# Kernel optimization log

Hardware: AMD Instinct MI355X
Metric: run time of the kernel (lower is better)

The kernel has to match this reference:

```python
import math
import jax, jax.numpy as jnp
import numpy as np

PS = 16   # patch_size
HD = 8    # hidden_dim in SigmaPredictor


def _bsp(x):
    # BoundedSoftplus(beta=1, threshold=6, eps=1e-6)
    return jnp.minimum(jax.nn.softplus(x), 6.0) + 1e-6


def _attn(q, k, v):
    s = jnp.einsum('bnd,bmd->bnm', q, k) * (HD ** -0.5)
    return jnp.einsum('bnm,bmd->bnd', jax.nn.softmax(s, axis=-1), v)


def _ln(x, g, b):
    mu = x.mean(-1, keepdims=True)
    var = ((x - mu) ** 2).mean(-1, keepdims=True)
    return (x - mu) / jnp.sqrt(var + 1e-5) * g + b


def _sigmas(x, Wq, bq, Wk, bk, Wv, bv, Wsq, bsq, Wsk, bsk, Wsv, bsv, ln_g, ln_b, Wp, bp):
    b, c, h, w = x.shape
    hp, wp = h // PS, w // PS
    # non-overlapping patchify -> [B, N, C*PS*PS]
    p = x.reshape(b, c, hp, PS, wp, PS).transpose(0, 2, 4, 1, 3, 5).reshape(b, hp * wp, c * PS * PS)
    feats = _attn(p @ Wq + bq, p @ Wk + bk, p @ Wv + bv)
    sp = _attn(feats @ Wsq + bsq, feats @ Wsk + bsk, feats @ Wsv + bsv)
    sp = _bsp(_ln(sp, ln_g, ln_b) @ Wp + bp)           # [B, N, 3]
    sp = sp.reshape(b, hp, wp, 3)
    # nearest-neighbor upsample by PS in both dims (exact match to F.interpolate 'nearest')
    return jnp.repeat(jnp.repeat(sp, PS, axis=1), PS, axis=2)  # [B,H,W,3]


def _filter(x, s, ksz):
    b, c, h, w = x.shape
    sx, sy, sr = s[..., 0], s[..., 1], s[..., 2]
    p = ksz // 2
    xp = jnp.pad(x, ((0, 0), (0, 0), (p, p), (p, p)), mode='reflect')
    # unfold -> [B, C, H, W, k*k], tap order (kh, kw) matches torch F.unfold
    patches = jnp.stack([xp[:, :, i:i + h, j:j + w] for i in range(ksz) for j in range(ksz)], axis=-1)
    offs = jnp.arange(-p, p + 1, dtype=x.dtype)
    yy, xx = jnp.meshgrid(offs, offs, indexing='ij')
    xxf, yyf = xx.reshape(-1), yy.reshape(-1)          # [k*k]
    spatial = jnp.exp(-(xxf ** 2 / (2 * sx[..., None] ** 2)
                        + yyf ** 2 / (2 * sy[..., None] ** 2)))  # [B,H,W,k*k]
    sq = ((x[..., None] - patches) ** 2).sum(axis=1, keepdims=True)  # [B,1,H,W,k*k]
    rng = jnp.exp(-sq / (2 * sr[:, None, :, :, None] ** 2))
    comb = spatial[:, None] * rng
    normk = comb / (comb.sum(-1, keepdims=True) + 1e-8)
    return (patches * normk).sum(-1)                   # [B,C,H,W]


def setup_inputs() -> dict:
    key = jax.random.key(0)
    ks = jax.random.split(key, 8)
    B, C, H, W = 2, 1, 512, 512
    Din = C * PS * PS

    def lin(k, i, o):
        return jax.random.normal(k, (i, o), jnp.float32) * 0.02

    return {
        'x': jax.random.normal(ks[0], (B, C, H, W), jnp.float32),
        'Wq': lin(ks[1], Din, HD), 'bq': jnp.zeros((HD,), jnp.float32),
        'Wk': lin(ks[2], Din, HD), 'bk': jnp.zeros((HD,), jnp.float32),
        'Wv': lin(ks[3], Din, HD), 'bv': jnp.zeros((HD,), jnp.float32),
        'Wsq': lin(ks[4], HD, HD), 'bsq': jnp.zeros((HD,), jnp.float32),
        'Wsk': lin(ks[5], HD, HD), 'bsk': jnp.zeros((HD,), jnp.float32),
        'Wsv': lin(ks[6], HD, HD), 'bsv': jnp.zeros((HD,), jnp.float32),
        'ln_g': jnp.ones((HD,), jnp.float32), 'ln_b': jnp.zeros((HD,), jnp.float32),
        'Wp': lin(ks[7], HD, 3),
        # bias sigma_proj so sigmas land ~[4.5,4.5,2.0] -> realistic k=11 window
        'bp': jnp.array([4.5, 4.5, 2.0], jnp.float32),
    }


def reference(x, Wq, bq, Wk, bk, Wv, bv, Wsq, bsq, Wsk, bsk, Wsv, bsv, ln_g, ln_b, Wp, bp):
    s = _sigmas(x, Wq, bq, Wk, bk, Wv, bv, Wsq, bsq, Wsk, bsk, Wsv, bsv, ln_g, ln_b, Wp, bp)
    # data-dependent kernel size (matches torch .item(); evaluated eagerly)
    m = float(jnp.maximum(s[..., 0].max(), s[..., 1].max()))
    k = int(2 * math.ceil(m) + 1)
    if k % 2 == 0:
        k += 1
    return _filter(x, s, k)
```

## Files before the change

kernel.cpp:

```cpp
#include <hip/hip_runtime.h>
#include <hip/hip_bf16.h>
#include <math.h>


#define B 2
#define N 1024
#define HW 512
#define IMG (HW*HW)

__global__ __launch_bounds__(256)
void qkv_kernel(const float* __restrict__ x,
                const float* __restrict__ Wq, const float* __restrict__ bq,
                const float* __restrict__ Wk, const float* __restrict__ bk,
                const float* __restrict__ Wv, const float* __restrict__ bv,
                float* __restrict__ Q, float* __restrict__ K, float* __restrict__ V,
                unsigned int* __restrict__ maxbits) {
    const int bn = blockIdx.x;
    const int b  = bn >> 10, n = bn & 1023;
    const int ph = n >> 5, pw = n & 31;
    const int tid = threadIdx.x;
    if (bn == 0 && tid == 0) atomicExch(maxbits, 0u);
    __shared__ float p[256];
    p[tid] = x[b * IMG + (ph * 16 + (tid >> 4)) * HW + pw * 16 + (tid & 15)];
    __syncthreads();
    if (tid < 192) {
        const int o = tid >> 3, sub = tid & 7;
        const int mat = o >> 3, j = o & 7;
        const float* W  = (mat == 0) ? Wq : (mat == 1) ? Wk : Wv;
        const float* bb = (mat == 0) ? bq : (mat == 1) ? bk : bv;
        float sum = 0.f;
#pragma unroll
        for (int dd = 0; dd < 32; ++dd) {
            const int d = dd * 8 + sub;
            sum = fmaf(p[d], W[d * 8 + j], sum);
        }
        sum += __shfl_xor(sum, 1);
        sum += __shfl_xor(sum, 2);
        sum += __shfl_xor(sum, 4);
        if (sub == 0) {
            float* op = (mat == 0) ? Q : (mat == 1) ? K : V;
            op[bn * 8 + j] = sum + bb[j];
        }
    }
}

__device__ __forceinline__ void attn_lds(const float* __restrict__ Qg,
                                         const float* __restrict__ Kb,
                                         const float* __restrict__ Vb,
                                         float* __restrict__ Kl, float* __restrict__ Vl,
                                         int qa, int qb, int tid, int lane,
                                         float fa[8], float fb[8]) {
    for (int i = tid; i < 2048; i += 256) {
        const float4 kv = ((const float4*)Kb)[i];
        const int tok = i >> 1, d0 = (i & 1) * 4;
        Kl[(d0 + 0) * 1024 + tok] = kv.x;
        Kl[(d0 + 1) * 1024 + tok] = kv.y;
        Kl[(d0 + 2) * 1024 + tok] = kv.z;
        Kl[(d0 + 3) * 1024 + tok] = kv.w;
        const float4 vv = ((const float4*)Vb)[i];
        Vl[(d0 + 0) * 1024 + tok] = vv.x;
        Vl[(d0 + 1) * 1024 + tok] = vv.y;
        Vl[(d0 + 2) * 1024 + tok] = vv.z;
        Vl[(d0 + 3) * 1024 + tok] = vv.w;
    }
    __syncthreads();

    float qav[8], qbv[8];
#pragma unroll
    for (int d = 0; d < 8; ++d) { qav[d] = Qg[qa * 8 + d]; qbv[d] = Qg[qb * 8 + d]; }

    const float SC = 0.35355339059327373f;
    const float L2E = 1.4426950408889634f;

    float mxa = -3.0e38f, mxb = -3.0e38f;
#pragma unroll
    for (int t = 0; t < 16; ++t) {
        const int tok = t * 64 + lane;
        float da = 0.f, db = 0.f;
#pragma unroll
        for (int d = 0; d < 8; ++d) {
            const float kd = Kl[d * 1024 + tok];
            da = fmaf(qav[d], kd, da);
            db = fmaf(qbv[d], kd, db);
        }
        mxa = fmaxf(mxa, da); mxb = fmaxf(mxb, db);
    }
#pragma unroll
    for (int off = 1; off < 64; off <<= 1) {
        mxa = fmaxf(mxa, __shfl_xor(mxa, off));
        mxb = fmaxf(mxb, __shfl_xor(mxb, off));
    }
    mxa *= SC; mxb *= SC;

    float sa = 0.f, sb = 0.f;
    float va[8] = {0,0,0,0,0,0,0,0}, vb[8] = {0,0,0,0,0,0,0,0};
#pragma unroll
    for (int t = 0; t < 16; ++t) {
        const int tok = t * 64 + lane;
        float da = 0.f, db = 0.f;
#pragma unroll
        for (int d = 0; d < 8; ++d) {
            const float kd = Kl[d * 1024 + tok];
            da = fmaf(qav[d], kd, da);
            db = fmaf(qbv[d], kd, db);
        }
        const float ea = exp2f((da * SC - mxa) * L2E);
        const float eb = exp2f((db * SC - mxb) * L2E);
        sa += ea; sb += eb;
#pragma unroll
        for (int d = 0; d < 8; ++d) {
            const float vd = Vl[d * 1024 + tok];
            va[d] = fmaf(ea, vd, va[d]);
            vb[d] = fmaf(eb, vd, vb[d]);
        }
    }
#pragma unroll
    for (int off = 1; off < 64; off <<= 1) {
        sa += __shfl_xor(sa, off);
        sb += __shfl_xor(sb, off);
#pragma unroll
        for (int d = 0; d < 8; ++d) {
            va[d] += __shfl_xor(va[d], off);
            vb[d] += __shfl_xor(vb[d], off);
        }
    }
    const float ia = 1.f / sa, ib = 1.f / sb;
#pragma unroll
    for (int d = 0; d < 8; ++d) { fa[d] = va[d] * ia; fb[d] = vb[d] * ib; }
}

__global__ __launch_bounds__(256)
void attn_proj_kernel(const float* __restrict__ Q, const float* __restrict__ K,
                      const float* __restrict__ V,
                      const float* __restrict__ Wsq, const float* __restrict__ bsq,
                      const float* __restrict__ Wsk, const float* __restrict__ bsk,
                      const float* __restrict__ Wsv, const float* __restrict__ bsv,
                      float* __restrict__ SQ, float* __restrict__ SK, float* __restrict__ SV) {
    __shared__ float Kl[8 * 1024];
    __shared__ float Vl[8 * 1024];
    const int tid = threadIdx.x, wid = tid >> 6, lane = tid & 63;
    const int q0 = blockIdx.x * 8;
    const int b  = q0 >> 10;
    const int qa = q0 + wid * 2, qb = qa + 1;
    float fa[8], fb[8];
    attn_lds(Q, K + (b << 13), V + (b << 13), Kl, Vl, qa, qb, tid, lane, fa, fb);
    const int sl = lane & 31;
    if (sl < 24) {
        const int mat = sl >> 3, j = sl & 7;
        const float* W  = (mat == 0) ? Wsq : (mat == 1) ? Wsk : Wsv;
        const float* bb = (mat == 0) ? bsq : (mat == 1) ? bsk : bsv;
        const float* f  = (lane < 32) ? fa : fb;
        const int bn    = (lane < 32) ? qa : qb;
        float o = bb[j];
#pragma unroll
        for (int d = 0; d < 8; ++d) o = fmaf(f[d], W[d * 8 + j], o);
        float* op = (mat == 0) ? SQ : (mat == 1) ? SK : SV;
        op[bn * 8 + j] = o;
    }
}

__global__ __launch_bounds__(256)
void attn_head_kernel(const float* __restrict__ SQ, const float* __restrict__ SK,
                      const float* __restrict__ SV,
                      const float* __restrict__ g, const float* __restrict__ be,
                      const float* __restrict__ Wp, const float* __restrict__ bp,
                      float* __restrict__ SP, unsigned int* __restrict__ maxbits) {
    __shared__ float Kl[8 * 1024];
    __shared__ float Vl[8 * 1024];
    const int tid = threadIdx.x, wid = tid >> 6, lane = tid & 63;
    const int q0 = blockIdx.x * 8;
    const int b  = q0 >> 10;
    const int qa = q0 + wid * 2, qb = qa + 1;
    float fa[8], fb[8];
    attn_lds(SQ, SK + (b << 13), SV + (b << 13), Kl, Vl, qa, qb, tid, lane, fa, fb);

    const float* f = (lane < 32) ? fa : fb;
    const int bn   = (lane < 32) ? qa : qb;
    float mu = 0.f;
#pragma unroll
    for (int d = 0; d < 8; ++d) mu += f[d];
    mu *= 0.125f;
    float var = 0.f;
#pragma unroll
    for (int d = 0; d < 8; ++d) { const float t = f[d] - mu; var = fmaf(t, t, var); }
    var *= 0.125f;
    const float inv = rsqrtf(var + 1e-5f);
    const int sl = lane & 31;
    float val = 0.f;
    if (sl < 3) {
        float o = bp[sl];
#pragma unroll
        for (int d = 0; d < 8; ++d) {
            const float nrm = (f[d] - mu) * inv * g[d] + be[d];
            o = fmaf(nrm, Wp[d * 3 + sl], o);
        }
        const float sp = fmaxf(o, 0.f) + log1pf(__expf(-fabsf(o)));
        const float v = fminf(sp, 6.0f) + 1e-6f;
        SP[bn * 3 + sl] = v;
        val = (sl < 2) ? v : 0.f;
    }
    float mv = val;
#pragma unroll
    for (int off = 1; off < 64; off <<= 1) mv = fmaxf(mv, __shfl_xor(mv, off));
    if (lane == 0) atomicMax(maxbits, __float_as_uint(mv));
}

template<int KK>
__device__ __forceinline__ void filt_spec(const float* __restrict__ xb, int h, int w,
                                          float nix, float niy, float nir,
                                          bool interiorBlk, float* __restrict__ out, int id) {
    constexpr int P = KK / 2;
    float ex[KK];
#pragma unroll
    for (int j = 0; j < KK; ++j) ex[j] = (float)((j - P) * (j - P)) * nix;
    const float xc = xb[h * HW + w];
    float acc0 = 0.f, ws0 = 0.f, acc1 = 0.f, ws1 = 0.f;
    if (interiorBlk) {
        const float* base = xb + (h - P) * HW + (w - P);
#pragma unroll
        for (int i = 0; i < KK; ++i) {
            const float eyr = (float)((i - P) * (i - P)) * niy;
            const float* row = base + i * HW;
#pragma unroll
            for (int j = 0; j < KK; ++j) {
                const float xv = row[j];
                const float dd = xc - xv;
                const float wg = exp2f(fmaf(dd * dd, nir, eyr + ex[j]));
                if (j & 1) { ws1 += wg; acc1 = fmaf(wg, xv, acc1); }
                else       { ws0 += wg; acc0 = fmaf(wg, xv, acc0); }
            }
        }
    } else {
#pragma unroll
        for (int i = 0; i < KK; ++i) {
            int row = h + i - P;
            row = (row < 0) ? -row : ((row > HW - 1) ? 2 * HW - 2 - row : row);
            const float eyr = (float)((i - P) * (i - P)) * niy;
            const float* rp = xb + row * HW;
#pragma unroll
            for (int j = 0; j < KK; ++j) {
                int col = w + j - P;
                col = (col < 0) ? -col : ((col > HW - 1) ? 2 * HW - 2 - col : col);
                const float xv = rp[col];
                const float dd = xc - xv;
                const float wg = exp2f(fmaf(dd * dd, nir, eyr + ex[j]));
                if (j & 1) { ws1 += wg; acc1 = fmaf(wg, xv, acc1); }
                else       { ws0 += wg; acc0 = fmaf(wg, xv, acc0); }
            }
        }
    }
    out[id] = (acc0 + acc1) / (ws0 + ws1 + 1e-8f);
}

__device__ void filt_generic(const float* __restrict__ xb, int h, int w, int kk,
                             float nix, float niy, float nir,
                             float* __restrict__ out, int id) {
    const int P = kk >> 1;
    const float xc = xb[h * HW + w];
    float acc = 0.f, wsum = 0.f;
    for (int i = 0; i < kk; ++i) {
        int row = h + i - P;
        row = (row < 0) ? -row : ((row > HW - 1) ? 2 * HW - 2 - row : row);
        const float eyr = (float)((i - P) * (i - P)) * niy;
        const float* rp = xb + row * HW;
        for (int j = 0; j < kk; ++j) {
            int col = w + j - P;
            col = (col < 0) ? -col : ((col > HW - 1) ? 2 * HW - 2 - col : col);
            const float xv = rp[col];
            const float dd = xc - xv;
            const float wg = exp2f(fmaf(dd * dd, nir, eyr + (float)((j - P) * (j - P)) * nix));
            wsum += wg;
            acc = fmaf(wg, xv, acc);
        }
    }
    out[id] = acc / (wsum + 1e-8f);
}

__global__ __launch_bounds__(256)
void filter_kernel(const float* __restrict__ x, const float* __restrict__ SP,
                   const unsigned int* __restrict__ maxbits, float* __restrict__ out) {
    const int blk = blockIdx.x;
    const int b = blk >> 10, n = blk & 1023;
    const int ph = n >> 5, pw = n & 31;
    const int tid = threadIdx.x;
    const int h = ph * 16 + (tid >> 4), w = pw * 16 + (tid & 15);
    const int id = b * IMG + h * HW + w;
    const float* xb = x + b * IMG;
    const float* sp = SP + (b * N + n) * 3;
    const float sx = sp[0], sy = sp[1], sr = sp[2];
    constexpr float L2E = 1.4426950408889634f;
    const float nix = -0.5f * L2E / (sx * sx);
    const float niy = -0.5f * L2E / (sy * sy);
    const float nir = -0.5f * L2E / (sr * sr);
    const float m = __uint_as_float(*maxbits);
    int kk = 2 * (int)ceilf(m) + 1;
    if (kk < 1) kk = 1;
    if (kk > 31) kk = 31;
    const bool ib = (ph > 0) & (ph < 31) & (pw > 0) & (pw < 31);
    if (kk == 11)      filt_spec<11>(xb, h, w, nix, niy, nir, ib, out, id);
    else if (kk == 9)  filt_spec<9>(xb, h, w, nix, niy, nir, ib, out, id);
    else if (kk == 13) filt_spec<13>(xb, h, w, nix, niy, nir, ib, out, id);
    else if (kk == 7)  filt_spec<7>(xb, h, w, nix, niy, nir, ib, out, id);
    else               filt_generic(xb, h, w, kk, nix, niy, nir, out, id);
}

extern "C" void kernel_launch(void* const* d_in, const int* in_sizes, int n_in,
                              void* d_out, int out_size, void* d_ws, size_t ws_size,
                              hipStream_t stream) {
    const float* x    = (const float*)d_in[0];
    const float* Wq   = (const float*)d_in[1];
    const float* bq   = (const float*)d_in[2];
    const float* Wk   = (const float*)d_in[3];
    const float* bk   = (const float*)d_in[4];
    const float* Wv   = (const float*)d_in[5];
    const float* bv   = (const float*)d_in[6];
    const float* Wsq  = (const float*)d_in[7];
    const float* bsq  = (const float*)d_in[8];
    const float* Wsk  = (const float*)d_in[9];
    const float* bsk  = (const float*)d_in[10];
    const float* Wsv  = (const float*)d_in[11];
    const float* bsv  = (const float*)d_in[12];
    const float* ln_g = (const float*)d_in[13];
    const float* ln_b = (const float*)d_in[14];
    const float* Wp   = (const float*)d_in[15];
    const float* bp   = (const float*)d_in[16];
    float* out = (float*)d_out;

    float* ws = (float*)d_ws;
    float* Q   = ws;
    float* Kf  = ws + 16384;
    float* Vf  = ws + 32768;
    float* SQ  = ws + 49152;
    float* SK  = ws + 65536;
    float* SV  = ws + 81920;
    float* SP  = ws + 98304;
    unsigned int* maxbits = (unsigned int*)(ws + 104448);

    qkv_kernel<<<B * N, 256, 0, stream>>>(x, Wq, bq, Wk, bk, Wv, bv, Q, Kf, Vf, maxbits);
    attn_proj_kernel<<<B * N / 8, 256, 0, stream>>>(Q, Kf, Vf, Wsq, bsq, Wsk, bsk, Wsv, bsv, SQ, SK, SV);
    attn_head_kernel<<<B * N / 8, 256, 0, stream>>>(SQ, SK, SV, ln_g, ln_b, Wp, bp, SP, maxbits);
    filter_kernel<<<B * N, 256, 0, stream>>>(x, SP, maxbits, out);
}
```

Measured before the change: 66.25 us.

## Compute four vertically adjacent output pixels per thread in bilateral filter

The filter kernel now gives each thread a column of four consecutive output rows inside a 32x32 tile per block. Each loaded input row of KK taps is held in registers and reused for every output pixel whose window covers it, so loads drop from 4*KK to KK+3 rows. The grid shrinks fourfold and register pressure per thread rises. The exp2 work is unchanged, so the gain depends on whether the kernel was limited by loads or by transcendental throughput.

```diff
diff --git a/kernel.cpp b/kernel.cpp
--- a/kernel.cpp
+++ b/kernel.cpp
@@ -206,86 +206,115 @@
 }
 
 template<int KK>
-__device__ __forceinline__ void filt_spec(const float* __restrict__ xb, int h, int w,
-                                          float nix, float niy, float nir,
-                                          bool interiorBlk, float* __restrict__ out, int id) {
+__device__ __forceinline__ void filt4(const float* __restrict__ xb, int r0, int w,
+                                      float nix, float niy, float nir,
+                                      bool interior, float* __restrict__ outb) {
     constexpr int P = KK / 2;
+    constexpr int RR = KK + 3;
     float ex[KK];
 #pragma unroll
     for (int j = 0; j < KK; ++j) ex[j] = (float)((j - P) * (j - P)) * nix;
-    const float xc = xb[h * HW + w];
-    float acc0 = 0.f, ws0 = 0.f, acc1 = 0.f, ws1 = 0.f;
-    if (interiorBlk) {
-        const float* base = xb + (h - P) * HW + (w - P);
-#pragma unroll
-        for (int i = 0; i < KK; ++i) {
-            const float eyr = (float)((i - P) * (i - P)) * niy;
-            const float* row = base + i * HW;
-#pragma unroll
-            for (int j = 0; j < KK; ++j) {
-                const float xv = row[j];
-                const float dd = xc - xv;
-                const float wg = exp2f(fmaf(dd * dd, nir, eyr + ex[j]));
-                if (j & 1) { ws1 += wg; acc1 = fmaf(wg, xv, acc1); }
-                else       { ws0 += wg; acc0 = fmaf(wg, xv, acc0); }
+    float xc[4], acc[4] = {0.f,0.f,0.f,0.f}, wsm[4] = {0.f,0.f,0.f,0.f};
+#pragma unroll
+    for (int p = 0; p < 4; ++p) xc[p] = xb[(r0 + p) * HW + w];
+    if (interior) {
+        const float* base = xb + (r0 - P) * HW + (w - P);
+#pragma unroll
+        for (int i = 0; i < RR; ++i) {
+            const float* rp = base + i * HW;
+            float rv[KK];
+#pragma unroll
+            for (int j = 0; j < KK; ++j) rv[j] = rp[j];
+#pragma unroll
+            for (int p = 0; p < 4; ++p) {
+                if (i >= p && i - p < KK) {
+                    const int di = i - p - P;
+                    const float eyr = (float)(di * di) * niy;
+#pragma unroll
+                    for (int j = 0; j < KK; ++j) {
+                        const float dd = xc[p] - rv[j];
+                        const float wg = exp2f(fmaf(dd * dd, nir, eyr + ex[j]));
+                        wsm[p] += wg;
+                        acc[p] = fmaf(wg, rv[j], acc[p]);
+                    }
+                }
             }
         }
     } else {
-#pragma unroll
-        for (int i = 0; i < KK; ++i) {
+        int cc[KK];
+#pragma unroll
+        for (int j = 0; j < KK; ++j) {
+            int c = w - P + j;
+            cc[j] = (c < 0) ? -c : ((c > HW - 1) ? 2 * HW - 2 - c : c);
+        }
+#pragma unroll
+        for (int i = 0; i < RR; ++i) {
+            int rr = r0 - P + i;
+            rr = (rr < 0) ? -rr : ((rr > HW - 1) ? 2 * HW - 2 - rr : rr);
+            const float* rp = xb + rr * HW;
+            float rv[KK];
+#pragma unroll
+            for (int j = 0; j < KK; ++j) rv[j] = rp[cc[j]];
+#pragma unroll
+            for (int p = 0; p < 4; ++p) {
+                if (i >= p && i - p < KK) {
+                    const int di = i - p - P;
+                    const float eyr = (float)(di * di) * niy;
+#pragma unroll
+                    for (int j = 0; j < KK; ++j) {
+                        const float dd = xc[p] - rv[j];
+                        const float wg = exp2f(fmaf(dd * dd, nir, eyr + ex[j]));
+                        wsm[p] += wg;
+                        acc[p] = fmaf(wg, rv[j], acc[p]);
+                    }
+                }
+            }
+        }
+    }
+#pragma unroll
+    for (int p = 0; p < 4; ++p)
+        outb[(r0 + p) * HW + w] = acc[p] / (wsm[p] + 1e-8f);
+}
+
+__device__ void filt4_generic(const float* __restrict__ xb, int r0, int w, int kk,
+                              float nix, float niy, float nir, float* __restrict__ outb) {
+    const int P = kk >> 1;
+    for (int p = 0; p < 4; ++p) {
+        const int h = r0 + p;
+        const float xcv = xb[h * HW + w];
+        float acc = 0.f, wsum = 0.f;
+        for (int i = 0; i < kk; ++i) {
             int row = h + i - P;
             row = (row < 0) ? -row : ((row > HW - 1) ? 2 * HW - 2 - row : row);
             const float eyr = (float)((i - P) * (i - P)) * niy;
             const float* rp = xb + row * HW;
-#pragma unroll
-            for (int j = 0; j < KK; ++j) {
+            for (int j = 0; j < kk; ++j) {
                 int col = w + j - P;
                 col = (col < 0) ? -col : ((col > HW - 1) ? 2 * HW - 2 - col : col);
                 const float xv = rp[col];
-                const float dd = xc - xv;
-                const float wg = exp2f(fmaf(dd * dd, nir, eyr + ex[j]));
-                if (j & 1) { ws1 += wg; acc1 = fmaf(wg, xv, acc1); }
-                else       { ws0 += wg; acc0 = fmaf(wg, xv, acc0); }
+                const float dd = xcv - xv;
+                const float wg = exp2f(fmaf(dd * dd, nir, eyr + (float)((j - P) * (j - P)) * nix));
+                wsum += wg;
+                acc = fmaf(wg, xv, acc);
             }
         }
-    }
-    out[id] = (acc0 + acc1) / (ws0 + ws1 + 1e-8f);
-}
-
-__device__ void filt_generic(const float* __restrict__ xb, int h, int w, int kk,
-                             float nix, float niy, float nir,
-                             float* __restrict__ out, int id) {
-    const int P = kk >> 1;
-    const float xc = xb[h * HW + w];
-    float acc = 0.f, wsum = 0.f;
-    for (int i = 0; i < kk; ++i) {
-        int row = h + i - P;
-        row = (row < 0) ? -row : ((row > HW - 1) ? 2 * HW - 2 - row : row);
-        const float eyr = (float)((i - P) * (i - P)) * niy;
-        const float* rp = xb + row * HW;
-        for (int j = 0; j < kk; ++j) {
-            int col = w + j - P;
-            col = (col < 0) ? -col : ((col > HW - 1) ? 2 * HW - 2 - col : col);
-            const float xv = rp[col];
-            const float dd = xc - xv;
-            const float wg = exp2f(fmaf(dd * dd, nir, eyr + (float)((j - P) * (j - P)) * nix));
-            wsum += wg;
-            acc = fmaf(wg, xv, acc);
-        }
-    }
-    out[id] = acc / (wsum + 1e-8f);
+        outb[h * HW + w] = acc / (wsum + 1e-8f);
+    }
 }
 
 __global__ __launch_bounds__(256)
 void filter_kernel(const float* __restrict__ x, const float* __restrict__ SP,
                    const unsigned int* __restrict__ maxbits, float* __restrict__ out) {
     const int blk = blockIdx.x;
-    const int b = blk >> 10, n = blk & 1023;
-    const int ph = n >> 5, pw = n & 31;
-    const int tid = threadIdx.x;
-    const int h = ph * 16 + (tid >> 4), w = pw * 16 + (tid & 15);
-    const int id = b * IMG + h * HW + w;
+    const int b = blk >> 8, t = blk & 255;
+    const int tr = t >> 4, tc = t & 15;
+    const int tx = threadIdx.x & 31;
+    const int ty = threadIdx.x >> 5;
+    const int w  = tc * 32 + tx;
+    const int r0 = tr * 32 + ty * 4;
+    const int n  = ((r0 >> 4) << 5) + (w >> 4);
     const float* xb = x + b * IMG;
+    float* outb = out + b * IMG;
     const float* sp = SP + (b * N + n) * 3;
     const float sx = sp[0], sy = sp[1], sr = sp[2];
     constexpr float L2E = 1.4426950408889634f;
@@ -296,12 +325,12 @@
     int kk = 2 * (int)ceilf(m) + 1;
     if (kk < 1) kk = 1;
     if (kk > 31) kk = 31;
-    const bool ib = (ph > 0) & (ph < 31) & (pw > 0) & (pw < 31);
-    if (kk == 11)      filt_spec<11>(xb, h, w, nix, niy, nir, ib, out, id);
-    else if (kk == 9)  filt_spec<9>(xb, h, w, nix, niy, nir, ib, out, id);
-    else if (kk == 13) filt_spec<13>(xb, h, w, nix, niy, nir, ib, out, id);
-    else if (kk == 7)  filt_spec<7>(xb, h, w, nix, niy, nir, ib, out, id);
-    else               filt_generic(xb, h, w, kk, nix, niy, nir, out, id);
+    const bool ib = (tr > 0) & (tr < 15) & (tc > 0) & (tc < 15);
+    if (kk == 11)      filt4<11>(xb, r0, w, nix, niy, nir, ib, outb);
+    else if (kk == 9)  filt4<9>(xb, r0, w, nix, niy, nir, ib, outb);
+    else if (kk == 13) filt4<13>(xb, r0, w, nix, niy, nir, ib, outb);
+    else if (kk == 7)  filt4<7>(xb, r0, w, nix, niy, nir, ib, outb);
+    else               filt4_generic(xb, r0, w, kk, nix, niy, nir, outb);
 }
 
 extern "C" void kernel_launch(void* const* d_in, const int* in_sizes, int n_in,
@@ -339,5 +368,5 @@
     qkv_kernel<<<B * N, 256, 0, stream>>>(x, Wq, bq, Wk, bk, Wv, bv, Q, Kf, Vf, maxbits);
     attn_proj_kernel<<<B * N / 8, 256, 0, stream>>>(Q, Kf, Vf, Wsq, bsq, Wsk, bsk, Wsv, bsv, SQ, SK, SV);
     attn_head_kernel<<<B * N / 8, 256, 0, stream>>>(SQ, SK, SV, ln_g, ln_b, Wp, bp, SP, maxbits);
-    filter_kernel<<<B * N, 256, 0, stream>>>(x, SP, maxbits, out);
-}
+    filter_kernel<<<B * 256, 256, 0, stream>>>(x, SP, maxbits, out);
+}
```

New measurement: 245.6 us. 3.71x slower.

## Split attention keys across 16 waves with flash-style merge and native exp2

Applied to the files above, without the earlier changes.

The two attention kernels now launch 1024 threads per block. Each group of four waves handles a quarter of the key tokens and caches the dot products in registers, so the second pass over K is dropped. Partial max, sum and V accumulators are merged through LDS with rescaling. exp2f is replaced by the native amdgcn exp2 builtin in the attention and bilateral filter loops, cutting the per-block serial work and exp cost at the price of extra barriers, LDS traffic and lower exp precision.

```diff
diff --git a/kernel.cpp b/kernel.cpp
--- a/kernel.cpp
+++ b/kernel.cpp
@@ -7,6 +7,14 @@
 #define N 1024
 #define HW 512
 #define IMG (HW*HW)
+
+__device__ __forceinline__ float fexp2(float x) {
+#if __has_builtin(__builtin_amdgcn_exp2f)
+    return __builtin_amdgcn_exp2f(x);
+#else
+    return exp2f(x);
+#endif
+}
 
 __global__ __launch_bounds__(256)
 void qkv_kernel(const float* __restrict__ x,
@@ -44,26 +52,40 @@
     }
 }
 
-__device__ __forceinline__ void attn_lds(const float* __restrict__ Qg,
-                                         const float* __restrict__ Kb,
-                                         const float* __restrict__ Vb,
-                                         float* __restrict__ Kl, float* __restrict__ Vl,
-                                         int qa, int qb, int tid, int lane,
-                                         float fa[8], float fb[8]) {
-    for (int i = tid; i < 2048; i += 256) {
+struct AttnLds {
+    float Kl[8 * 1024];
+    float Vl[8 * 1024];
+    float pm[4][4][2];
+    float ps[4][4][2];
+    float pv[4][4][2][8];
+    float ff[8][8];
+    float mr[8];
+};
+
+__device__ __forceinline__ void attn_core(AttnLds& S,
+                                          const float* __restrict__ Qg,
+                                          const float* __restrict__ Kb,
+                                          const float* __restrict__ Vb,
+                                          int q0, int tid) {
+    for (int i = tid; i < 2048; i += 1024) {
         const float4 kv = ((const float4*)Kb)[i];
         const int tok = i >> 1, d0 = (i & 1) * 4;
-        Kl[(d0 + 0) * 1024 + tok] = kv.x;
-        Kl[(d0 + 1) * 1024 + tok] = kv.y;
-        Kl[(d0 + 2) * 1024 + tok] = kv.z;
-        Kl[(d0 + 3) * 1024 + tok] = kv.w;
+        S.Kl[(d0 + 0) * 1024 + tok] = kv.x;
+        S.Kl[(d0 + 1) * 1024 + tok] = kv.y;
+        S.Kl[(d0 + 2) * 1024 + tok] = kv.z;
+        S.Kl[(d0 + 3) * 1024 + tok] = kv.w;
         const float4 vv = ((const float4*)Vb)[i];
-        Vl[(d0 + 0) * 1024 + tok] = vv.x;
-        Vl[(d0 + 1) * 1024 + tok] = vv.y;
-        Vl[(d0 + 2) * 1024 + tok] = vv.z;
-        Vl[(d0 + 3) * 1024 + tok] = vv.w;
-    }
-    __syncthreads();
+        S.Vl[(d0 + 0) * 1024 + tok] = vv.x;
+        S.Vl[(d0 + 1) * 1024 + tok] = vv.y;
+        S.Vl[(d0 + 2) * 1024 + tok] = vv.z;
+        S.Vl[(d0 + 3) * 1024 + tok] = vv.w;
+    }
+    __syncthreads();
+
+    const int w = tid >> 6, lane = tid & 63;
+    const int p = w & 3, tq = w >> 2;
+    const int qa = q0 + p * 2, qb = qa + 1;
+    const int tok0 = tq * 256;
 
     float qav[8], qbv[8];
 #pragma unroll
@@ -72,17 +94,19 @@
     const float SC = 0.35355339059327373f;
     const float L2E = 1.4426950408889634f;
 
+    float dA[4], dB[4];
     float mxa = -3.0e38f, mxb = -3.0e38f;
 #pragma unroll
-    for (int t = 0; t < 16; ++t) {
-        const int tok = t * 64 + lane;
+    for (int t = 0; t < 4; ++t) {
+        const int tok = tok0 + t * 64 + lane;
         float da = 0.f, db = 0.f;
 #pragma unroll
         for (int d = 0; d < 8; ++d) {
-            const float kd = Kl[d * 1024 + tok];
+            const float kd = S.Kl[d * 1024 + tok];
             da = fmaf(qav[d], kd, da);
             db = fmaf(qbv[d], kd, db);
         }
+        dA[t] = da; dB[t] = db;
         mxa = fmaxf(mxa, da); mxb = fmaxf(mxb, db);
     }
 #pragma unroll
@@ -95,21 +119,14 @@
     float sa = 0.f, sb = 0.f;
     float va[8] = {0,0,0,0,0,0,0,0}, vb[8] = {0,0,0,0,0,0,0,0};
 #pragma unroll
-    for (int t = 0; t < 16; ++t) {
-        const int tok = t * 64 + lane;
-        float da = 0.f, db = 0.f;
+    for (int t = 0; t < 4; ++t) {
+        const int tok = tok0 + t * 64 + lane;
+        const float ea = fexp2((dA[t] * SC - mxa) * L2E);
+        const float eb = fexp2((dB[t] * SC - mxb) * L2E);
+        sa += ea; sb += eb;
 #pragma unroll
         for (int d = 0; d < 8; ++d) {
-            const float kd = Kl[d * 1024 + tok];
-            da = fmaf(qav[d], kd, da);
-            db = fmaf(qbv[d], kd, db);
-        }
-        const float ea = exp2f((da * SC - mxa) * L2E);
-        const float eb = exp2f((db * SC - mxb) * L2E);
-        sa += ea; sb += eb;
-#pragma unroll
-        for (int d = 0; d < 8; ++d) {
-            const float vd = Vl[d * 1024 + tok];
+            const float vd = S.Vl[d * 1024 + tok];
             va[d] = fmaf(ea, vd, va[d]);
             vb[d] = fmaf(eb, vd, vb[d]);
         }
@@ -124,85 +141,108 @@
             vb[d] += __shfl_xor(vb[d], off);
         }
     }
-    const float ia = 1.f / sa, ib = 1.f / sb;
-#pragma unroll
-    for (int d = 0; d < 8; ++d) { fa[d] = va[d] * ia; fb[d] = vb[d] * ib; }
-}
-
-__global__ __launch_bounds__(256)
+    if (lane == 0) {
+        S.pm[p][tq][0] = mxa; S.pm[p][tq][1] = mxb;
+        S.ps[p][tq][0] = sa;  S.ps[p][tq][1] = sb;
+#pragma unroll
+        for (int d = 0; d < 8; ++d) {
+            S.pv[p][tq][0][d] = va[d];
+            S.pv[p][tq][1][d] = vb[d];
+        }
+    }
+    __syncthreads();
+
+    if (tid < 8) {
+        const int pidx = tid >> 1, which = tid & 1;
+        float m = S.pm[pidx][0][which];
+#pragma unroll
+        for (int t = 1; t < 4; ++t) m = fmaxf(m, S.pm[pidx][t][which]);
+        float s = 0.f, vd[8] = {0,0,0,0,0,0,0,0};
+#pragma unroll
+        for (int t = 0; t < 4; ++t) {
+            const float f = fexp2((S.pm[pidx][t][which] - m) * L2E);
+            s = fmaf(S.ps[pidx][t][which], f, s);
+#pragma unroll
+            for (int d = 0; d < 8; ++d)
+                vd[d] = fmaf(S.pv[pidx][t][which][d], f, vd[d]);
+        }
+        const float inv = 1.f / s;
+#pragma unroll
+        for (int d = 0; d < 8; ++d) S.ff[tid][d] = vd[d] * inv;
+    }
+    __syncthreads();
+}
+
+__global__ __launch_bounds__(1024)
 void attn_proj_kernel(const float* __restrict__ Q, const float* __restrict__ K,
                       const float* __restrict__ V,
                       const float* __restrict__ Wsq, const float* __restrict__ bsq,
                       const float* __restrict__ Wsk, const float* __restrict__ bsk,
                       const float* __restrict__ Wsv, const float* __restrict__ bsv,
                       float* __restrict__ SQ, float* __restrict__ SK, float* __restrict__ SV) {
-    __shared__ float Kl[8 * 1024];
-    __shared__ float Vl[8 * 1024];
-    const int tid = threadIdx.x, wid = tid >> 6, lane = tid & 63;
+    __shared__ AttnLds S;
+    const int tid = threadIdx.x;
     const int q0 = blockIdx.x * 8;
     const int b  = q0 >> 10;
-    const int qa = q0 + wid * 2, qb = qa + 1;
-    float fa[8], fb[8];
-    attn_lds(Q, K + (b << 13), V + (b << 13), Kl, Vl, qa, qb, tid, lane, fa, fb);
-    const int sl = lane & 31;
-    if (sl < 24) {
-        const int mat = sl >> 3, j = sl & 7;
+    attn_core(S, Q, K + (b << 13), V + (b << 13), q0, tid);
+    if (tid < 192) {
+        const int q = tid / 24, o = tid - q * 24;
+        const int mat = o >> 3, j = o & 7;
         const float* W  = (mat == 0) ? Wsq : (mat == 1) ? Wsk : Wsv;
         const float* bb = (mat == 0) ? bsq : (mat == 1) ? bsk : bsv;
-        const float* f  = (lane < 32) ? fa : fb;
-        const int bn    = (lane < 32) ? qa : qb;
-        float o = bb[j];
-#pragma unroll
-        for (int d = 0; d < 8; ++d) o = fmaf(f[d], W[d * 8 + j], o);
+        float s = bb[j];
+#pragma unroll
+        for (int d = 0; d < 8; ++d) s = fmaf(S.ff[q][d], W[d * 8 + j], s);
         float* op = (mat == 0) ? SQ : (mat == 1) ? SK : SV;
-        op[bn * 8 + j] = o;
-    }
-}
-
-__global__ __launch_bounds__(256)
+        op[(q0 + q) * 8 + j] = s;
+    }
+}
+
+__global__ __launch_bounds__(1024)
 void attn_head_kernel(const float* __restrict__ SQ, const float* __restrict__ SK,
                       const float* __restrict__ SV,
                       const float* __restrict__ g, const float* __restrict__ be,
                       const float* __restrict__ Wp, const float* __restrict__ bp,
                       float* __restrict__ SP, unsigned int* __restrict__ maxbits) {
-    __shared__ float Kl[8 * 1024];
-    __shared__ float Vl[8 * 1024];
-    const int tid = threadIdx.x, wid = tid >> 6, lane = tid & 63;
+    __shared__ AttnLds S;
+    const int tid = threadIdx.x;
     const int q0 = blockIdx.x * 8;
     const int b  = q0 >> 10;
-    const int qa = q0 + wid * 2, qb = qa + 1;
-    float fa[8], fb[8];
-    attn_lds(SQ, SK + (b << 13), SV + (b << 13), Kl, Vl, qa, qb, tid, lane, fa, fb);
-
-    const float* f = (lane < 32) ? fa : fb;
-    const int bn   = (lane < 32) ? qa : qb;
-    float mu = 0.f;
-#pragma unroll
-    for (int d = 0; d < 8; ++d) mu += f[d];
-    mu *= 0.125f;
-    float var = 0.f;
-#pragma unroll
-    for (int d = 0; d < 8; ++d) { const float t = f[d] - mu; var = fmaf(t, t, var); }
-    var *= 0.125f;
-    const float inv = rsqrtf(var + 1e-5f);
-    const int sl = lane & 31;
-    float val = 0.f;
-    if (sl < 3) {
-        float o = bp[sl];
-#pragma unroll
-        for (int d = 0; d < 8; ++d) {
-            const float nrm = (f[d] - mu) * inv * g[d] + be[d];
-            o = fmaf(nrm, Wp[d * 3 + sl], o);
-        }
-        const float sp = fmaxf(o, 0.f) + log1pf(__expf(-fabsf(o)));
-        const float v = fminf(sp, 6.0f) + 1e-6f;
-        SP[bn * 3 + sl] = v;
-        val = (sl < 2) ? v : 0.f;
-    }
-    float mv = val;
-#pragma unroll
-    for (int off = 1; off < 64; off <<= 1) mv = fmaxf(mv, __shfl_xor(mv, off));
-    if (lane == 0) atomicMax(maxbits, __float_as_uint(mv));
+    attn_core(S, SQ, SK + (b << 13), SV + (b << 13), q0, tid);
+    if (tid < 8) {
+        const float* f = S.ff[tid];
+        float mu = 0.f;
+#pragma unroll
+        for (int d = 0; d < 8; ++d) mu += f[d];
+        mu *= 0.125f;
+        float var = 0.f;
+#pragma unroll
+        for (int d = 0; d < 8; ++d) { const float t = f[d] - mu; var = fmaf(t, t, var); }
+        var *= 0.125f;
+        const float inv = rsqrtf(var + 1e-5f);
+        float mloc = 0.f;
+#pragma unroll
+        for (int l = 0; l < 3; ++l) {
+            float o = bp[l];
+#pragma unroll
+            for (int d = 0; d < 8; ++d) {
+                const float nrm = (f[d] - mu) * inv * g[d] + be[d];
+                o = fmaf(nrm, Wp[d * 3 + l], o);
+            }
+            const float sp = fmaxf(o, 0.f) + log1pf(__expf(-fabsf(o)));
+            const float v = fminf(sp, 6.0f) + 1e-6f;
+            SP[(q0 + tid) * 3 + l] = v;
+            if (l < 2) mloc = fmaxf(mloc, v);
+        }
+        S.mr[tid] = mloc;
+    }
+    __syncthreads();
+    if (tid == 0) {
+        float m = S.mr[0];
+#pragma unroll
+        for (int i = 1; i < 8; ++i) m = fmaxf(m, S.mr[i]);
+        atomicMax(maxbits, __float_as_uint(m));
+    }
 }
 
 template<int KK>
@@ -225,7 +265,7 @@
             for (int j = 0; j < KK; ++j) {
                 const float xv = row[j];
                 const float dd = xc - xv;
-                const float wg = exp2f(fmaf(dd * dd, nir, eyr + ex[j]));
+                const float wg = fexp2(fmaf(dd * dd, nir, eyr + ex[j]));
                 if (j & 1) { ws1 += wg; acc1 = fmaf(wg, xv, acc1); }
                 else       { ws0 += wg; acc0 = fmaf(wg, xv, acc0); }
             }
@@ -243,7 +283,7 @@
                 col = (col < 0) ? -col : ((col > HW - 1) ? 2 * HW - 2 - col : col);
                 const float xv = rp[col];
                 const float dd = xc - xv;
-                const float wg = exp2f(fmaf(dd * dd, nir, eyr + ex[j]));
+                const float wg = fexp2(fmaf(dd * dd, nir, eyr + ex[j]));
                 if (j & 1) { ws1 += wg; acc1 = fmaf(wg, xv, acc1); }
                 else       { ws0 += wg; acc0 = fmaf(wg, xv, acc0); }
             }
@@ -268,7 +308,7 @@
             col = (col < 0) ? -col : ((col > HW - 1) ? 2 * HW - 2 - col : col);
             const float xv = rp[col];
             const float dd = xc - xv;
-            const float wg = exp2f(fmaf(dd * dd, nir, eyr + (float)((j - P) * (j - P)) * nix));
+            const float wg = fexp2(fmaf(dd * dd, nir, eyr + (float)((j - P) * (j - P)) * nix));
             wsum += wg;
             acc = fmaf(wg, xv, acc);
         }
@@ -337,7 +377,7 @@
     unsigned int* maxbits = (unsigned int*)(ws + 104448);
 
     qkv_kernel<<<B * N, 256, 0, stream>>>(x, Wq, bq, Wk, bk, Wv, bv, Q, Kf, Vf, maxbits);
-    attn_proj_kernel<<<B * N / 8, 256, 0, stream>>>(Q, Kf, Vf, Wsq, bsq, Wsk, bsk, Wsv, bsv, SQ, SK, SV);
-    attn_head_kernel<<<B * N / 8, 256, 0, stream>>>(SQ, SK, SV, ln_g, ln_b, Wp, bp, SP, maxbits);
+    attn_proj_kernel<<<B * N / 8, 1024, 0, stream>>>(Q, Kf, Vf, Wsq, bsq, Wsk, bsk, Wsv, bsv, SQ, SK, SV);
+    attn_head_kernel<<<B * N / 8, 1024, 0, stream>>>(SQ, SK, SV, ln_g, ln_b, Wp, bp, SP, maxbits);
     filter_kernel<<<B * N, 256, 0, stream>>>(x, SP, maxbits, out);
 }
```

Measured after the change: 55.67 us. -16.0%, faster.
